# Kernel optimization log

Hardware: AMD Instinct MI355X
Metric: run time of the kernel (lower is better)

## Reference

```python
import jax, jax.numpy as jnp
import numpy as np

N_NODES, N_EDGES, F_IN, F_OUT = 10000, 320000, 256, 256


def setup_inputs() -> dict:
    key = jax.random.key(0)
    k1, k2, k3, k4, k5, k6 = jax.random.split(key, 6)
    feature = jax.random.normal(k1, (N_NODES, F_IN), jnp.float32)
    ew = jax.random.uniform(k2, (N_EDGES,), jnp.float32)          # edge weights
    src = jax.random.randint(k3, (N_EDGES,), 0, N_NODES)
    dst = jax.random.randint(k4, (N_EDGES,), 0, N_NODES)
    # nn.Linear(2*in_feats, out_feats): weight [out, 2*in], bias [out]
    W = jax.random.normal(k5, (F_OUT, 2 * F_IN), jnp.float32) / np.sqrt(2 * F_IN)
    b = jax.random.normal(k6, (F_OUT,), jnp.float32) * 0.01
    return {"feature": feature, "ew": ew, "src": src, "dst": dst, "W": W, "b": b}


def reference(feature, ew, src, dst, W, b):
    n = feature.shape[0]
    # edge_msg2: m[e] = h[src[0]] * h[src[e]] * w[e]   -> [E, F]
    msg = feature[src[0]] * feature[src] * ew[:, None]
    # reduce: segment mean over incoming edges (mailbox mean). The original
    # reduce also computes a segment max concatenated into 'hm', but the apply
    # module only consumes the mean half ('hm_mean', Linear in = 2*in_feats),
    # so the max is dead compute and omitted.
    sums = jax.ops.segment_sum(msg, dst, num_segments=n)
    cnt = jax.ops.segment_sum(jnp.ones((msg.shape[0],), msg.dtype), dst, num_segments=n)
    hm_mean = sums / jnp.maximum(cnt, 1.0)[:, None]
    # NodeApplyModule: relu(Linear(cat(h, hm_mean)))
    x = jnp.concatenate([feature, hm_mean], axis=1)  # [N, 2F]
    return jax.nn.relu(x @ W.T + b)
```

## Files before the change

### kernel.cpp

```cpp
#include <hip/hip_runtime.h>

#define N_NODES 10000
#define N_EDGES 320000
#define F 256
#define K2 512
#define HSLOT 48
#define SLOTS 96
#define CSTR 16
#define W_BLOCKS 128
#define ZCNT_BLOCKS 313
#define K0_BLOCKS (W_BLOCKS + ZCNT_BLOCKS)
#define K1_BLOCKS 4375
#define N_TILE16 625

typedef __attribute__((ext_vector_type(8))) __bf16 bf16x8;
typedef __attribute__((ext_vector_type(4))) __bf16 bf16x4;
typedef __attribute__((ext_vector_type(4))) float f32x4;
typedef __attribute__((ext_vector_type(2))) float f32x2;
typedef unsigned long long u64;
typedef unsigned int u32;
typedef unsigned short u16;


__global__ __launch_bounds__(256) void prep_kernel(
    const float* __restrict__ feat,
    const float* __restrict__ Wm,
    const int* __restrict__ src,
    __bf16* __restrict__ Wt,
    int* __restrict__ cnt) {
  int b = blockIdx.x;
  int tid = threadIdx.x;
  if (b < W_BLOCKS) {
    int idx = b * 256 + tid;
    int o_ = idx >> 7;
    int k = (idx & 127) * 4;
    float4 w = ((const float4*)Wm)[idx];
    if (k >= F) {
      int s0 = src[0];
      float4 h = ((const float4*)(feat + (size_t)s0 * F))[(k - F) >> 2];
      w.x *= h.x; w.y *= h.y; w.z *= h.z; w.w *= h.w;
    }
    bf16x4 o;
    o[0] = (__bf16)w.x; o[1] = (__bf16)w.y; o[2] = (__bf16)w.z; o[3] = (__bf16)w.w;
    int t = k >> 5, kq = (k & 31) >> 3, e = k & 7;
    size_t offT = (((size_t)t * 4 + kq) * 256 + o_) * 8 + e;
    *(bf16x4*)(Wt + offT) = o;
  } else {
    int idx = (b - W_BLOCKS) * 256 + tid;
    if (idx < 2 * N_NODES * CSTR / 4) ((int4*)cnt)[idx] = make_int4(0, 0, 0, 0);
  }
}

__global__ __launch_bounds__(256) void mega_kernel(
    const float* __restrict__ feat,
    const int* __restrict__ src,
    const int* __restrict__ dst,
    const float* __restrict__ ew,
    int* __restrict__ cnt,
    u32* __restrict__ bucket,
    u32* __restrict__ feat8,
    const __bf16* __restrict__ Wt,
    const float* __restrict__ bias,
    float* __restrict__ out) {
  int b = blockIdx.x;
  int tid = threadIdx.x;
  int g = b / 7;
  int r = b % 7;
  if (r == 0 || r == 3) {
    int sid = g * 2 + (r == 3);
    int e = sid * 256 + tid;
    if (e >= N_EDGES) return;
    int d = dst[e];
    int par = e & 1;
    u32 wb = (__float_as_uint(ew[e]) + 0x8000u) & 0xFFFF0000u;
    int p = atomicAdd(&cnt[(d * 2 + par) * CSTR], 1);
    if (p < HSLOT) bucket[(size_t)d * SLOTS + par * HSLOT + p] = wb | (u32)src[e];
  } else if (r == 6) {
    int mt = g;
    const int wave = tid >> 6;
    const int lane = tid & 63;
    const int r15 = lane & 15;
    const int kq = lane >> 4;
    const int col0 = wave * 64;
    const int m0 = mt * 16;
    const float* arow = feat + (size_t)(m0 + r15) * F;

    f32x4 acc[4];
#pragma unroll
    for (int cs = 0; cs < 4; ++cs) acc[cs] = (f32x4){0.f, 0.f, 0.f, 0.f};

#pragma unroll
    for (int t = 0; t < 8; ++t) {
      float4 lo = *(const float4*)(arow + t * 32 + kq * 8);
      float4 hi = *(const float4*)(arow + t * 32 + kq * 8 + 4);
      bf16x8 a;
      a[0] = (__bf16)lo.x; a[1] = (__bf16)lo.y; a[2] = (__bf16)lo.z; a[3] = (__bf16)lo.w;
      a[4] = (__bf16)hi.x; a[5] = (__bf16)hi.y; a[6] = (__bf16)hi.z; a[7] = (__bf16)hi.w;
#pragma unroll
      for (int cs = 0; cs < 4; ++cs) {
        bf16x8 bb = *(const bf16x8*)(Wt + (((size_t)t * 4 + kq) * 256 + col0 + cs * 16 + r15) * 8);
        acc[cs] = __builtin_amdgcn_mfma_f32_16x16x32_bf16(a, bb, acc[cs], 0, 0, 0);
      }
    }

    const int rbase = kq * 4;
#pragma unroll
    for (int cs = 0; cs < 4; ++cs) {
      int col = col0 + cs * 16 + r15;
      float bv = bias[col];
#pragma unroll
      for (int r2 = 0; r2 < 4; ++r2) {
        int orow = m0 + rbase + r2;
        out[(size_t)orow * F + col] = acc[cs][r2] + bv;
      }
    }
  } else {
    int ci = (r < 3) ? (r - 1) : (r - 2);
    int idx = (g * 4 + ci) * 256 + tid;
    float4 v = ((const float4*)feat)[idx];
    u32 r8 = 0;
    r8 = __builtin_amdgcn_cvt_pk_fp8_f32(v.x, v.y, r8, false);
    r8 = __builtin_amdgcn_cvt_pk_fp8_f32(v.z, v.w, r8, true);
    feat8[idx] = r8;
  }
}

__global__ __launch_bounds__(256) void node_agg_kernel(
    const u32* __restrict__ feat8,
    const u32* __restrict__ bucket,
    const int* __restrict__ cnt,
    __bf16* __restrict__ aggb) {
  int node = (blockIdx.x * 256 + threadIdx.x) >> 6;
  int lane = threadIdx.x & 63;
  if (node >= N_NODES) return;
  int c0 = cnt[(node * 2) * CSTR];
  int c1 = cnt[(node * 2 + 1) * CSTR];
  int cc0 = min(c0, HSLOT);
  int cc1 = min(c1, HSLOT);
  int cc = cc0 + cc1;
  int c = c0 + c1;
  const u32* bk = bucket + (size_t)node * SLOTS;
  const uint2* frow = (const uint2*)feat8;
  const int half = lane >> 5;
  const int slot = lane & 31;

  f32x2 a01 = {0.f, 0.f}, a23 = {0.f, 0.f}, a45 = {0.f, 0.f}, a67 = {0.f, 0.f};

  int i = 0;
  for (; i + 16 <= cc; i += 16) {
    u32 p[8];
    uint2 v[8];
#pragma unroll
    for (int j = 0; j < 8; ++j) {
      int e = i + half + 2 * j;
      int si = (e < cc0) ? e : (e - cc0 + HSLOT);
      p[j] = bk[si];
    }
#pragma unroll
    for (int j = 0; j < 8; ++j)
      v[j] = frow[(size_t)(p[j] & 0xFFFFu) * 32 + slot];
#pragma unroll
    for (int j = 0; j < 8; ++j) {
      float w = __uint_as_float(p[j] & 0xFFFF0000u);
      f32x2 w2 = {w, w};
      a01 += __builtin_amdgcn_cvt_pk_f32_fp8(v[j].x, false) * w2;
      a23 += __builtin_amdgcn_cvt_pk_f32_fp8(v[j].x, true) * w2;
      a45 += __builtin_amdgcn_cvt_pk_f32_fp8(v[j].y, false) * w2;
      a67 += __builtin_amdgcn_cvt_pk_f32_fp8(v[j].y, true) * w2;
    }
  }
  if (i < cc) {
    u32 p[8];
    uint2 v[8];
#pragma unroll
    for (int j = 0; j < 8; ++j) {
      int e = i + half + 2 * j;
      int ec = min(e, cc - 1);
      int si = (ec < cc0) ? ec : (ec - cc0 + HSLOT);
      p[j] = bk[si];
    }
#pragma unroll
    for (int j = 0; j < 8; ++j)
      v[j] = frow[(size_t)(p[j] & 0xFFFFu) * 32 + slot];
#pragma unroll
    for (int j = 0; j < 8; ++j) {
      int e = i + half + 2 * j;
      float w = (e < cc) ? __uint_as_float(p[j] & 0xFFFF0000u) : 0.f;
      f32x2 w2 = {w, w};
      a01 += __builtin_amdgcn_cvt_pk_f32_fp8(v[j].x, false) * w2;
      a23 += __builtin_amdgcn_cvt_pk_f32_fp8(v[j].x, true) * w2;
      a45 += __builtin_amdgcn_cvt_pk_f32_fp8(v[j].y, false) * w2;
      a67 += __builtin_amdgcn_cvt_pk_f32_fp8(v[j].y, true) * w2;
    }
  }

  float acc[8] = {a01[0], a01[1], a23[0], a23[1], a45[0], a45[1], a67[0], a67[1]};
#pragma unroll
  for (int e = 0; e < 8; ++e) acc[e] += __shfl_xor(acc[e], 32, 64);

  if (half == 0) {
    float ic = 1.0f / (float)max(c, 1);
    bf16x8 o;
#pragma unroll
    for (int e = 0; e < 8; ++e) o[e] = (__bf16)(acc[e] * ic);
    *(bf16x8*)(aggb + (size_t)node * F + slot * 8) = o;
  }
}

__global__ __launch_bounds__(256) void gemmB_kernel(
    const __bf16* __restrict__ aggb,
    const __bf16* __restrict__ Wt,
    float* __restrict__ out) {
  const int tid = threadIdx.x;
  const int wave = tid >> 6;
  const int lane = tid & 63;
  const int r15 = lane & 15;
  const int kq = lane >> 4;
  const int col0 = wave * 64;
  const int m0 = blockIdx.x * 16;

  const __bf16* arow = aggb + (size_t)(m0 + r15) * F;

  f32x4 acc[4];
#pragma unroll
  for (int cs = 0; cs < 4; ++cs) acc[cs] = (f32x4){0.f, 0.f, 0.f, 0.f};

#pragma unroll
  for (int t2 = 0; t2 < 8; ++t2) {
    bf16x8 a = *(const bf16x8*)(arow + t2 * 32 + kq * 8);
#pragma unroll
    for (int cs = 0; cs < 4; ++cs) {
      bf16x8 bb = *(const bf16x8*)(Wt + (((size_t)(t2 + 8) * 4 + kq) * 256 + col0 + cs * 16 + r15) * 8);
      acc[cs] = __builtin_amdgcn_mfma_f32_16x16x32_bf16(a, bb, acc[cs], 0, 0, 0);
    }
  }

  const int rbase = kq * 4;
#pragma unroll
  for (int cs = 0; cs < 4; ++cs) {
    int col = col0 + cs * 16 + r15;
#pragma unroll
    for (int r = 0; r < 4; ++r) {
      int orow = m0 + rbase + r;
      size_t oi = (size_t)orow * F + col;
      out[oi] = fmaxf(out[oi] + acc[cs][r], 0.0f);
    }
  }
}

extern "C" void kernel_launch(void* const* d_in, const int* in_sizes, int n_in,
                              void* d_out, int out_size, void* d_ws, size_t ws_size,
                              hipStream_t stream) {
  const float* feat = (const float*)d_in[0];
  const float* ew   = (const float*)d_in[1];
  const int*   src  = (const int*)d_in[2];
  const int*   dst  = (const int*)d_in[3];
  const float* Wm   = (const float*)d_in[4];
  const float* bias = (const float*)d_in[5];
  float* out = (float*)d_out;

  u32*    bucket = (u32*)d_ws;
  __bf16* aggb   = (__bf16*)(bucket + (size_t)N_NODES * SLOTS);
  __bf16* Wt     = aggb + (size_t)N_NODES * F;
  u32*    feat8  = (u32*)(Wt + (size_t)F * K2);
  int*    cnt    = (int*)(feat8 + (size_t)N_NODES * F / 4);

  prep_kernel<<<K0_BLOCKS, 256, 0, stream>>>(feat, Wm, src, Wt, cnt);
  mega_kernel<<<K1_BLOCKS, 256, 0, stream>>>(feat, src, dst, ew, cnt, bucket,
                                             feat8, Wt, bias, out);
  node_agg_kernel<<<(N_NODES * 64 + 255) / 256, 256, 0, stream>>>(feat8, bucket, cnt, aggb);
  gemmB_kernel<<<N_TILE16, 256, 0, stream>>>(aggb, Wt, out);
}
```

Measured before the change: 53.69 us.

## Split node aggregation and overlap second half with first-half GEMM tiles

Splits node aggregation into two halves across two launches. The second launch runs aggregation for the upper nodes alongside the GEMM-B tiles for the lower nodes, whose aggregated rows were finished by the first launch. A final launch handles the remaining GEMM-B tiles. The aim is to cut tail and idle time between the aggregation and GEMM phases by overlapping them, at the cost of one extra kernel launch.

After: 58.64 us. 1.09x slower.

```diff
diff --git a/kernel.cpp b/kernel.cpp
--- a/kernel.cpp
+++ b/kernel.cpp
@@ -11,7 +11,12 @@
 #define ZCNT_BLOCKS 313
 #define K0_BLOCKS (W_BLOCKS + ZCNT_BLOCKS)
 #define K1_BLOCKS 4375
-#define N_TILE16 625
+#define SPLIT_N 4992
+#define AGG1_BLOCKS 1248
+#define AGG2_BLOCKS 1252
+#define GB1_TILES 312
+#define K2B_BLOCKS (AGG2_BLOCKS + GB1_TILES)
+#define GB2_TILES 313
 
 typedef __attribute__((ext_vector_type(8))) __bf16 bf16x8;
 typedef __attribute__((ext_vector_type(4))) __bf16 bf16x4;
@@ -125,14 +130,11 @@
   }
 }
 
-__global__ __launch_bounds__(256) void node_agg_kernel(
-    const u32* __restrict__ feat8,
-    const u32* __restrict__ bucket,
-    const int* __restrict__ cnt,
-    __bf16* __restrict__ aggb) {
-  int node = (blockIdx.x * 256 + threadIdx.x) >> 6;
-  int lane = threadIdx.x & 63;
-  if (node >= N_NODES) return;
+__device__ inline void do_agg_node(int node, int lane,
+                                   const u32* __restrict__ feat8,
+                                   const u32* __restrict__ bucket,
+                                   const int* __restrict__ cnt,
+                                   __bf16* __restrict__ aggb) {
   int c0 = cnt[(node * 2) * CSTR];
   int c1 = cnt[(node * 2 + 1) * CSTR];
   int cc0 = min(c0, HSLOT);
@@ -207,17 +209,16 @@
   }
 }
 
-__global__ __launch_bounds__(256) void gemmB_kernel(
-    const __bf16* __restrict__ aggb,
-    const __bf16* __restrict__ Wt,
-    float* __restrict__ out) {
-  const int tid = threadIdx.x;
+__device__ inline void do_gemmB_tile(int mt, int tid,
+                                     const __bf16* __restrict__ aggb,
+                                     const __bf16* __restrict__ Wt,
+                                     float* __restrict__ out) {
   const int wave = tid >> 6;
   const int lane = tid & 63;
   const int r15 = lane & 15;
   const int kq = lane >> 4;
   const int col0 = wave * 64;
-  const int m0 = blockIdx.x * 16;
+  const int m0 = mt * 16;
 
   const __bf16* arow = aggb + (size_t)(m0 + r15) * F;
 
@@ -246,6 +247,40 @@
       out[oi] = fmaxf(out[oi] + acc[cs][r], 0.0f);
     }
   }
+}
+
+__global__ __launch_bounds__(256) void agg1_kernel(
+    const u32* __restrict__ feat8,
+    const u32* __restrict__ bucket,
+    const int* __restrict__ cnt,
+    __bf16* __restrict__ aggb) {
+  int node = (blockIdx.x * 256 + threadIdx.x) >> 6;
+  if (node >= SPLIT_N) return;
+  do_agg_node(node, threadIdx.x & 63, feat8, bucket, cnt, aggb);
+}
+
+__global__ __launch_bounds__(256) void agg2_gemmB1_kernel(
+    const u32* __restrict__ feat8,
+    const u32* __restrict__ bucket,
+    const int* __restrict__ cnt,
+    __bf16* __restrict__ aggb,
+    const __bf16* __restrict__ Wt,
+    float* __restrict__ out) {
+  int b = blockIdx.x;
+  if (b < AGG2_BLOCKS) {
+    int node = SPLIT_N + ((b * 256 + threadIdx.x) >> 6);
+    if (node >= N_NODES) return;
+    do_agg_node(node, threadIdx.x & 63, feat8, bucket, cnt, aggb);
+  } else {
+    do_gemmB_tile(b - AGG2_BLOCKS, threadIdx.x, aggb, Wt, out);
+  }
+}
+
+__global__ __launch_bounds__(256) void gemmB2_kernel(
+    const __bf16* __restrict__ aggb,
+    const __bf16* __restrict__ Wt,
+    float* __restrict__ out) {
+  do_gemmB_tile(GB1_TILES + blockIdx.x, threadIdx.x, aggb, Wt, out);
 }
 
 extern "C" void kernel_launch(void* const* d_in, const int* in_sizes, int n_in,
@@ -268,6 +303,7 @@
   prep_kernel<<<K0_BLOCKS, 256, 0, stream>>>(feat, Wm, src, Wt, cnt);
   mega_kernel<<<K1_BLOCKS, 256, 0, stream>>>(feat, src, dst, ew, cnt, bucket,
                                              feat8, Wt, bias, out);
-  node_agg_kernel<<<(N_NODES * 64 + 255) / 256, 256, 0, stream>>>(feat8, bucket, cnt, aggb);
-  gemmB_kernel<<<N_TILE16, 256, 0, stream>>>(aggb, Wt, out);
-}
+  agg1_kernel<<<AGG1_BLOCKS, 256, 0, stream>>>(feat8, bucket, cnt, aggb);
+  agg2_gemmB1_kernel<<<K2B_BLOCKS, 256, 0, stream>>>(feat8, bucket, cnt, aggb, Wt, out);
+  gemmB2_kernel<<<GB2_TILES, 256, 0, stream>>>(aggb, Wt, out);
+}
```
